# Performance work log

Hardware: AMD Instinct MI355X
Metric: run time of the kernel (lower is better)

The kernel has to match this reference:

```python
import jax, jax.numpy as jnp
import numpy as np

B, S, HID = 2, 4096, 3584
NH, NKV, HD, FD = 16, 8, 256, 64
CHUNK = 64

def _rope_tables(seq_len, dim, base=10000.0):
    inv = 1.0 / (base ** (np.arange(0, dim, 2) / dim))      # [dim/2]
    f = np.outer(np.arange(seq_len), inv)                   # [S, dim/2]
    return jnp.asarray(np.cos(f), jnp.float32), jnp.asarray(np.sin(f), jnp.float32)

def setup_inputs() -> dict:
    key = jax.random.key(0)
    ks = jax.random.split(key, 8)
    def w(k, shape, fan):
        return jax.random.normal(k, shape, jnp.float32) * (fan ** -0.5)
    cos, sin = _rope_tables(S, HD)
    return dict(
        hidden_states=jax.random.normal(ks[0], (B, S, HID), jnp.float32),
        cos=cos, sin=sin,
        Wq=w(ks[1], (HID, NH * HD), HID),
        Wk=w(ks[2], (HID, NKV * HD), HID),
        Wv=w(ks[3], (HID, NKV * HD), HID),
        Wo=w(ks[4], (NH * HD, HID), NH * HD),
        fmq=w(ks[5], (NH, HD, FD), HD),
        fmk=w(ks[6], (NH, HD, FD), HD),
    )

def apply_rope(x, cos, sin):
    # Gemma split-half rotary. x: [B,S,h,D]; cos/sin: [S,D/2]
    d2 = x.shape[-1] // 2
    x1, x2 = x[..., :d2], x[..., d2:]
    c = cos[None, :, None, :]
    s = sin[None, :, None, :]
    return jnp.concatenate([x1 * c - x2 * s, x1 * s + x2 * c], axis=-1)

def feature_map(x, w):
    # Hedgehog: per-head linear then cat(softmax(z), softmax(-z)).
    # x: [B,h,S,D], w: [h,D,F] -> [B,h,S,2F]
    z = jnp.einsum('bhsd,hdf->bhsf', x, w)
    return jnp.concatenate([jax.nn.softmax(z, axis=-1), jax.nn.softmax(-z, axis=-1)], axis=-1)

def chunk_linear_attn(q, k, v, chunk=CHUNK):
    # q,k: [B,H,T,dk]; v: [B,H,T,dv]; T divisible by chunk (S=4096, chunk=64)
    b, h, T, dk = q.shape
    dv = v.shape[-1]
    n = T // chunk
    q = q.reshape(b, h, n, chunk, dk) * (dk ** -0.5)
    k = k.reshape(b, h, n, chunk, dk)
    v = v.reshape(b, h, n, chunk, dv)
    kv = jnp.einsum('bhncd,bhnce->bhnde', k, v)          # per-chunk K^T V: [b,h,n,dk,dv]
    kv = jnp.cumsum(kv, axis=2)
    kv = jnp.concatenate([jnp.zeros_like(kv[:, :, :1]), kv[:, :, :-1]], axis=2)  # exclusive
    inter = jnp.einsum('bhncd,bhnde->bhnce', q, kv)
    scores = jnp.einsum('bhncd,bhnkd->bhnck', q, k)
    causal = jnp.tril(jnp.ones((chunk, chunk), dtype=bool))
    scores = jnp.where(causal, scores, jnp.zeros((), scores.dtype))
    intra = jnp.einsum('bhnck,bhnke->bhnce', scores, v)
    return (inter + intra).reshape(b, h, T, dv)

def reference(hidden_states, cos, sin, Wq, Wk, Wv, Wo, fmq, fmk):
    b, s, _ = hidden_states.shape
    q = (hidden_states @ Wq).reshape(b, s, NH, HD)
    k = (hidden_states @ Wk).reshape(b, s, NKV, HD)
    v = (hidden_states @ Wv).reshape(b, s, NKV, HD)
    q = apply_rope(q, cos, sin)
    k = apply_rope(k, cos, sin)
    g = NH // NKV
    k = jnp.repeat(k, g, axis=2)   # GQA expansion
    v = jnp.repeat(v, g, axis=2)
    q = q.transpose(0, 2, 1, 3)    # [B,H,S,D]
    k = k.transpose(0, 2, 1, 3)
    v = v.transpose(0, 2, 1, 3)
    q = feature_map(q, fmq)        # [B,H,S,2F]
    k = feature_map(k, fmk)
    o = chunk_linear_attn(q, k, v)                      # [B,H,S,HD]
    o = o.transpose(0, 2, 1, 3).reshape(b, s, NH * HD)
    return o @ Wo
```

## Files before the change

kernel.cpp:

```cpp
#include <hip/hip_runtime.h>

typedef float  f32x4  __attribute__((ext_vector_type(4)));
typedef __bf16 bf16x4 __attribute__((ext_vector_type(4)));
typedef __bf16 bf16x8 __attribute__((ext_vector_type(8)));

#define MFMA16(a,b,c) __builtin_amdgcn_mfma_f32_16x16x32_bf16((a),(b),(c),0,0,0)

__device__ __forceinline__ void async_copy16(void* lds, const void* gmem) {
  __builtin_amdgcn_global_load_lds(
      (const __attribute__((address_space(1))) void*)gmem,
      (__attribute__((address_space(3))) void*)lds, 16, 0, 0);
}

template<int N> __device__ __forceinline__ void vmcnt_gate() {
  if constexpr (N == 8) asm volatile("s_waitcnt vmcnt(8)" ::: "memory");
  else if constexpr (N == 4) asm volatile("s_waitcnt vmcnt(4)" ::: "memory");
  else if constexpr (N == 0) asm volatile("s_waitcnt vmcnt(0)" ::: "memory");
}

__global__ __launch_bounds__(256) void convert_kernel(const float* __restrict__ in,
                                                      __bf16* __restrict__ out, size_t n4) {
  size_t i = (size_t)blockIdx.x * 256 + threadIdx.x;
  if (i >= n4) return;
  f32x4 v = *(const f32x4*)(in + i * 4);
  bf16x4 o;
  #pragma unroll
  for (int j = 0; j < 4; ++j) o[j] = (__bf16)v[j];
  *(bf16x4*)(out + i * 4) = o;
}

__global__ __launch_bounds__(256) void transpose_kernel(const float* __restrict__ in,
                                                        __bf16* __restrict__ out, int R, int C) {
  __shared__ float tile[32][33];
  int bx = blockIdx.x, by = blockIdx.y;
  int tx = threadIdx.x & 31, ty0 = threadIdx.x >> 5;
  #pragma unroll
  for (int i = 0; i < 4; ++i) {
    int r = by * 32 + ty0 + i * 8;
    tile[ty0 + i * 8][tx] = in[(size_t)r * C + bx * 32 + tx];
  }
  __syncthreads();
  #pragma unroll
  for (int i = 0; i < 4; ++i) {
    int c = bx * 32 + ty0 + i * 8;
    out[(size_t)c * R + by * 32 + tx] = (__bf16)tile[tx][ty0 + i * 8];
  }
}


__device__ __forceinline__ void stage_q(__bf16* region, int qrow, const __bf16* src,
                                        int K, int w, int l) {
  int r = qrow + w * 8 + (l >> 3);
  async_copy16(region + (size_t)(qrow + w * 8) * 64,
               src + (size_t)r * K + (((l & 7) ^ (r & 7)) << 3));
}

#define PH_SYNC_PRE  do { asm volatile("s_barrier" ::: "memory"); \
                          asm volatile("s_waitcnt lgkmcnt(0)" ::: "memory"); \
                          __builtin_amdgcn_sched_barrier(0); \
                          __builtin_amdgcn_s_setprio(1); } while (0)
#define PH_SYNC_POST do { __builtin_amdgcn_s_setprio(0); \
                          __builtin_amdgcn_sched_barrier(0); } while (0)

template<bool LATE, bool EARLY, int GATE>
__device__ __forceinline__ void tile_body(__bf16* smem,
                                          const __bf16* Apan, const __bf16* Bpan,
                                          int K, int tau, int wm, int wn,
                                          int lo, int hi, int w, int l,
                                          f32x4 (&acc)[8][4]) {
  const int buf = tau & 1, nbuf = buf ^ 1;
  __bf16* Ab = smem + buf * 32768;
  __bf16* Bb = Ab + 16384;
  __bf16* An = smem + nbuf * 32768;
  __bf16* Bn = An + 16384;
  bf16x8 a[4], b[4];

  #pragma unroll
  for (int t = 0; t < 4; ++t) {
    int ra = wm * 128 + t * 16 + lo;
    a[t] = *(const bf16x8*)(Ab + (size_t)ra * 64 + ((hi ^ (ra & 7)) << 3));
  }
  #pragma unroll
  for (int t = 0; t < 4; ++t) {
    int rb = wn * 64 + t * 16 + lo;
    b[t] = *(const bf16x8*)(Bb + (size_t)rb * 64 + ((hi ^ (rb & 7)) << 3));
  }
  if constexpr (LATE) {
    const __bf16* Ap1 = Apan + (size_t)(tau + 1) * 64;
    const __bf16* Bp1 = Bpan + (size_t)(tau + 1) * 64;
    stage_q(An, 64,  Ap1, K, w, l);
    stage_q(An, 192, Ap1, K, w, l);
    stage_q(Bn, 128, Bp1, K, w, l);
    stage_q(Bn, 192, Bp1, K, w, l);
  }
  PH_SYNC_PRE;
  #pragma unroll
  for (int mt = 0; mt < 4; ++mt)
    #pragma unroll
    for (int nt = 0; nt < 4; ++nt)
      acc[mt][nt] = MFMA16(a[mt], b[nt], acc[mt][nt]);
  PH_SYNC_POST;
  asm volatile("s_barrier" ::: "memory");

  #pragma unroll
  for (int t = 0; t < 4; ++t) {
    int ra = wm * 128 + 64 + t * 16 + lo;
    a[t] = *(const bf16x8*)(Ab + (size_t)ra * 64 + ((hi ^ (ra & 7)) << 3));
  }
  PH_SYNC_PRE;
  #pragma unroll
  for (int mt = 0; mt < 4; ++mt)
    #pragma unroll
    for (int nt = 0; nt < 4; ++nt)
      acc[4 + mt][nt] = MFMA16(a[mt], b[nt], acc[4 + mt][nt]);
  PH_SYNC_POST;
  asm volatile("s_barrier" ::: "memory");

  #pragma unroll
  for (int t = 0; t < 4; ++t) {
    int ra = wm * 128 + t * 16 + lo;
    a[t] = *(const bf16x8*)(Ab + (size_t)ra * 64 + (((4 + hi) ^ (ra & 7)) << 3));
  }
  #pragma unroll
  for (int t = 0; t < 4; ++t) {
    int rb = wn * 64 + t * 16 + lo;
    b[t] = *(const bf16x8*)(Bb + (size_t)rb * 64 + (((4 + hi) ^ (rb & 7)) << 3));
  }
  PH_SYNC_PRE;
  #pragma unroll
  for (int mt = 0; mt < 4; ++mt)
    #pragma unroll
    for (int nt = 0; nt < 4; ++nt)
      acc[mt][nt] = MFMA16(a[mt], b[nt], acc[mt][nt]);
  PH_SYNC_POST;
  asm volatile("s_barrier" ::: "memory");

  #pragma unroll
  for (int t = 0; t < 4; ++t) {
    int ra = wm * 128 + 64 + t * 16 + lo;
    a[t] = *(const bf16x8*)(Ab + (size_t)ra * 64 + (((4 + hi) ^ (ra & 7)) << 3));
  }
  if constexpr (EARLY) {
    const __bf16* Ap2 = Apan + (size_t)(tau + 2) * 64;
    const __bf16* Bp2 = Bpan + (size_t)(tau + 2) * 64;
    stage_q(Ab, 0,   Ap2, K, w, l);
    stage_q(Ab, 128, Ap2, K, w, l);
    stage_q(Bb, 0,   Bp2, K, w, l);
    stage_q(Bb, 64,  Bp2, K, w, l);
  }
  PH_SYNC_PRE;
  #pragma unroll
  for (int mt = 0; mt < 4; ++mt)
    #pragma unroll
    for (int nt = 0; nt < 4; ++nt)
      acc[4 + mt][nt] = MFMA16(a[mt], b[nt], acc[4 + mt][nt]);
  PH_SYNC_POST;
  vmcnt_gate<GATE>();
  asm volatile("s_barrier" ::: "memory");
}

template <typename CT>
__global__ __launch_bounds__(512) void gemm256_kernel(const __bf16* __restrict__ A,
                                                      const __bf16* __restrict__ Bt,
                                                      CT* __restrict__ C, int M, int N, int K) {
  extern __shared__ __bf16 smem[];

  const int gx = gridDim.x;
  const int nwg = gx * gridDim.y;
  const int wg = blockIdx.y * gx + blockIdx.x;
  const int qq = nwg >> 3;
  const int id2 = (wg & 7) * qq + (wg >> 3);
  const int m0 = (id2 / gx) * 256, n0 = (id2 % gx) * 256;

  const int tid = threadIdx.x;
  const int l = tid & 63, w = tid >> 6;
  const int lo = l & 15, hi = l >> 4;
  const int wm = w >> 2, wn = w & 3;

  const __bf16* Apan = A + (size_t)m0 * K;
  const __bf16* Bpan = Bt + (size_t)n0 * K;

  f32x4 acc[8][4] = {};

  #pragma unroll
  for (int q = 0; q < 4; ++q) stage_q(smem,          q * 64, Apan,      K, w, l);
  #pragma unroll
  for (int q = 0; q < 4; ++q) stage_q(smem + 16384,  q * 64, Bpan,      K, w, l);
  #pragma unroll
  for (int q = 0; q < 4; ++q) stage_q(smem + 32768,  q * 64, Apan + 64, K, w, l);
  #pragma unroll
  for (int q = 0; q < 4; ++q) stage_q(smem + 49152,  q * 64, Bpan + 64, K, w, l);
  asm volatile("s_waitcnt vmcnt(8)" ::: "memory");
  asm volatile("s_barrier" ::: "memory");

  const int T = K >> 6;
  tile_body<false, true, 4>(smem, Apan, Bpan, K, 0, wm, wn, lo, hi, w, l, acc);
  for (int tau = 1; tau < T - 2; ++tau)
    tile_body<true, true, 4>(smem, Apan, Bpan, K, tau, wm, wn, lo, hi, w, l, acc);
  tile_body<true, false, 0>(smem, Apan, Bpan, K, T - 2, wm, wn, lo, hi, w, l, acc);
  tile_body<false, false, -1>(smem, Apan, Bpan, K, T - 1, wm, wn, lo, hi, w, l, acc);

  #pragma unroll
  for (int mt = 0; mt < 8; ++mt)
    #pragma unroll
    for (int nt = 0; nt < 4; ++nt) {
      int col = n0 + wn * 64 + nt * 16 + lo;
      #pragma unroll
      for (int r = 0; r < 4; ++r) {
        int row = m0 + wm * 128 + mt * 16 + 4 * hi + r;
        C[(size_t)row * N + col] = (CT)acc[mt][nt][r];
      }
    }
}

__global__ __launch_bounds__(256) void rope_kernel(const __bf16* __restrict__ qin,
                                                   const float* __restrict__ cosT,
                                                   const float* __restrict__ sinT,
                                                   __bf16* __restrict__ outp, int H, int bshift) {
  int idx = blockIdx.x * 256 + threadIdx.x;
  int j = idx & 31;
  int s = (idx >> 5) & 4095;
  int h = (idx >> 17) & (H - 1);
  int b = idx >> bshift;
  int d = j * 4;
  size_t ibase = ((size_t)(b * 4096 + s)) * (H * 256) + h * 256 + d;
  bf16x4 x1 = *(const bf16x4*)&qin[ibase];
  bf16x4 x2 = *(const bf16x4*)&qin[ibase + 128];
  f32x4 c  = *(const f32x4*)&cosT[s * 128 + d];
  f32x4 sn = *(const f32x4*)&sinT[s * 128 + d];
  bf16x4 o1, o2;
  #pragma unroll
  for (int t = 0; t < 4; ++t) {
    float a = (float)x1[t], bb = (float)x2[t];
    o1[t] = (__bf16)(a * c[t] - bb * sn[t]);
    o2[t] = (__bf16)(a * sn[t] + bb * c[t]);
  }
  size_t obase = (((size_t)(b * H + h)) * 4096 + s) * 256 + d;
  *(bf16x4*)&outp[obase] = o1;
  *(bf16x4*)&outp[obase + 128] = o2;
}

__global__ __launch_bounds__(256) void vperm_kernel(const __bf16* __restrict__ in,
                                                    __bf16* __restrict__ out) {
  int idx = blockIdx.x * 256 + threadIdx.x;
  int j = idx & 31;
  int s = (idx >> 5) & 4095;
  int kv = (idx >> 17) & 7;
  int b = idx >> 20;
  bf16x8 v = *(const bf16x8*)&in[((size_t)(b * 4096 + s)) * 2048 + kv * 256 + j * 8];
  *(bf16x8*)&out[(((size_t)(b * 8 + kv)) * 4096 + s) * 256 + j * 8] = v;
}

__global__ __launch_bounds__(256) void fm_kernel(const __bf16* __restrict__ rope,
                                                 const float* __restrict__ fm,
                                                 __bf16* __restrict__ out, int srcH, float scale) {
  __shared__ __bf16 fmT[64][256];
  int bh = blockIdx.y;
  int h = bh & 15, b = bh >> 4;
  int s0 = blockIdx.x * 128;
  int tid = threadIdx.x, lane = tid & 63, wid = tid >> 6, hi = lane >> 4, lo = lane & 15;

  const float* fmh = fm + (size_t)h * 256 * 64;
  for (int i = tid; i < 256 * 64; i += 256) {
    int d = i >> 6, f = i & 63;
    fmT[f][(((d >> 3) ^ (f & 7)) << 3) | (d & 7)] = (__bf16)fmh[i];
  }
  __syncthreads();

  int srch = (srcH == 16) ? h : (h >> 1);
  const __bf16* abase = rope + ((size_t)(b * srcH + srch) * 4096 + s0 + 32 * wid) * 256;
  f32x4 acc[2][4] = {};
  for (int kk = 0; kk < 256; kk += 32) {
    bf16x8 a[2], bf[4];
    #pragma unroll
    for (int mt = 0; mt < 2; ++mt)
      a[mt] = *(const bf16x8*)(abase + (size_t)(16 * mt + lo) * 256 + kk + 8 * hi);
    const int G = (kk >> 3) + hi;
    #pragma unroll
    for (int nt = 0; nt < 4; ++nt) {
      int f = 16 * nt + lo;
      bf[nt] = *(const bf16x8*)&fmT[f][(G ^ (f & 7)) << 3];
    }
    #pragma unroll
    for (int mt = 0; mt < 2; ++mt)
      #pragma unroll
      for (int nt = 0; nt < 4; ++nt)
        acc[mt][nt] = MFMA16(a[mt], bf[nt], acc[mt][nt]);
  }

  size_t obase = ((size_t)(b * 16 + h) * 4096 + s0 + 32 * wid);
  #pragma unroll
  for (int mt = 0; mt < 2; ++mt) {
    #pragma unroll
    for (int r = 0; r < 4; ++r) {
      float z0 = acc[mt][0][r], z1 = acc[mt][1][r], z2 = acc[mt][2][r], z3 = acc[mt][3][r];
      float mx = fmaxf(fmaxf(z0, z1), fmaxf(z2, z3));
      float mn = fminf(fminf(z0, z1), fminf(z2, z3));
      #pragma unroll
      for (int off = 1; off < 16; off <<= 1) {
        mx = fmaxf(mx, __shfl_xor(mx, off));
        mn = fminf(mn, __shfl_xor(mn, off));
      }
      float ep0 = __expf(z0 - mx), ep1 = __expf(z1 - mx), ep2 = __expf(z2 - mx), ep3 = __expf(z3 - mx);
      float en0 = __expf(mn - z0), en1 = __expf(mn - z1), en2 = __expf(mn - z2), en3 = __expf(mn - z3);
      float sp = ep0 + ep1 + ep2 + ep3, sn = en0 + en1 + en2 + en3;
      #pragma unroll
      for (int off = 1; off < 16; off <<= 1) {
        sp += __shfl_xor(sp, off);
        sn += __shfl_xor(sn, off);
      }
      float rp = scale / sp, rn = scale / sn;
      int row = 16 * mt + 4 * hi + r;
      __bf16* op = out + (obase + row) * 128;
      op[0  + lo] = (__bf16)(ep0 * rp);  op[16 + lo] = (__bf16)(ep1 * rp);
      op[32 + lo] = (__bf16)(ep2 * rp);  op[48 + lo] = (__bf16)(ep3 * rp);
      op[64 + lo] = (__bf16)(en0 * rn);  op[80 + lo] = (__bf16)(en1 * rn);
      op[96 + lo] = (__bf16)(en2 * rn);  op[112 + lo] = (__bf16)(en3 * rn);
    }
  }
}

__global__ __launch_bounds__(256) void attn_kernel(const __bf16* __restrict__ qf,
                                                   const __bf16* __restrict__ kf,
                                                   const __bf16* __restrict__ vp,
                                                   __bf16* __restrict__ o) {
  __shared__ __bf16 k_s[64][128];
  __shared__ __bf16 vT_s[32][64];
  __shared__ __bf16 sc_s[64][64];
  __shared__ __bf16 STb[32][128];

  int bid = blockIdx.x;
  int dvb = bid & 7, h = (bid >> 3) & 15, b = bid >> 7;
  int dv0 = dvb * 32;
  int tid = threadIdx.x, lane = tid & 63, wid = tid >> 6, hi = lane >> 4, lo = lane & 15;

  const __bf16* qh = qf + ((size_t)(b * 16 + h)) * 4096 * 128;
  const __bf16* kh = kf + ((size_t)(b * 16 + h)) * 4096 * 128;
  const __bf16* vh = vp + ((size_t)(b * 8 + (h >> 1))) * 4096 * 256 + dv0;
  __bf16* oh = o + ((size_t)b * 4096) * 4096 + h * 256 + dv0;

  {
    unsigned int* z = (unsigned int*)&STb[0][0];
    for (int i = tid; i < 2048; i += 256) z[i] = 0u;
  }
  f32x4 st[2][2] = {};

  for (int n = 0; n < 64; ++n) {
    int s0 = n * 64;
    #pragma unroll
    for (int i = 0; i < 4; ++i) {
      int rb = (wid * 4 + i) * 4;
      int r = rb + (lane >> 4);
      int Glog = (lane & 15) ^ (r & 7);
      async_copy16(&k_s[rb][0], kh + (size_t)(s0 + r) * 128 + Glog * 8);
    }
    {
      int c = tid >> 2, d8 = (tid & 3) * 8;
      bf16x8 vv = *(const bf16x8*)(vh + (size_t)(s0 + c) * 256 + d8);
      #pragma unroll
      for (int j = 0; j < 8; ++j) {
        int dv = d8 + j;
        vT_s[dv][(((c >> 3) ^ (dv & 7)) << 3) | (c & 7)] = vv[j];
      }
    }
    __syncthreads();

    bf16x8 aq[4];
    #pragma unroll
    for (int kq = 0; kq < 4; ++kq)
      aq[kq] = *(const bf16x8*)(qh + (size_t)(s0 + 16 * wid + lo) * 128 + 32 * kq + 8 * hi);

    f32x4 acc_o[2] = {}, sacc[4] = {};
    #pragma unroll
    for (int nt = 0; nt < 2; ++nt)
      #pragma unroll
      for (int kq = 0; kq < 4; ++kq) {
        int rr = 16 * nt + lo, G = 4 * kq + hi;
        bf16x8 bf = *(const bf16x8*)&STb[rr][(G ^ (rr & 7)) << 3];
        acc_o[nt] = MFMA16(aq[kq], bf, acc_o[nt]);
      }
    #pragma unroll
    for (int nt = 0; nt < 4; ++nt)
      #pragma unroll
      for (int kq = 0; kq < 4; ++kq) {
        int rr = 16 * nt + lo, G = 4 * kq + hi;
        bf16x8 bf = *(const bf16x8*)&k_s[rr][(G ^ (rr & 7)) << 3];
        sacc[nt] = MFMA16(aq[kq], bf, sacc[nt]);
      }
    #pragma unroll
    for (int nt = 0; nt < 4; ++nt)
      #pragma unroll
      for (int r = 0; r < 4; ++r) {
        int c = 16 * wid + 4 * hi + r;
        int cp = 16 * nt + lo;
        float v = (cp <= c) ? sacc[nt][r] : 0.0f;
        sc_s[c][(((cp >> 3) ^ (c & 7)) << 3) | (cp & 7)] = (__bf16)v;
      }
    asm volatile("" ::: "memory");
    #pragma unroll
    for (int nt = 0; nt < 2; ++nt)
      #pragma unroll
      for (int kq = 0; kq < 2; ++kq) {
        int rA = 16 * wid + lo, GA = 4 * kq + hi;
        bf16x8 af = *(const bf16x8*)&sc_s[rA][(GA ^ (rA & 7)) << 3];
        int rB = 16 * nt + lo;
        bf16x8 bf = *(const bf16x8*)&vT_s[rB][(GA ^ (rB & 7)) << 3];
        acc_o[nt] = MFMA16(af, bf, acc_o[nt]);
      }
    #pragma unroll
    for (int nt = 0; nt < 2; ++nt)
      #pragma unroll
      for (int r = 0; r < 4; ++r) {
        int c = 16 * wid + 4 * hi + r;
        oh[(size_t)(s0 + c) * 4096 + 16 * nt + lo] = (__bf16)acc_o[nt][r];
      }
    __syncthreads();

    bf16x8 bu[2][2];
    #pragma unroll
    for (int q = 0; q < 2; ++q) {
      int dk = 16 * (2 * wid + q) + lo;
      #pragma unroll
      for (int kq = 0; kq < 2; ++kq) {
        bf16x8 tmp;
        #pragma unroll
        for (int j = 0; j < 8; ++j) {
          int c = 32 * kq + 8 * hi + j;
          tmp[j] = k_s[c][(((dk >> 3) ^ (c & 7)) << 3) | (dk & 7)];
        }
        bu[q][kq] = tmp;
      }
    }
    #pragma unroll
    for (int mt = 0; mt < 2; ++mt)
      #pragma unroll
      for (int kq = 0; kq < 2; ++kq) {
        int rA = 16 * mt + lo, GA = 4 * kq + hi;
        bf16x8 av = *(const bf16x8*)&vT_s[rA][(GA ^ (rA & 7)) << 3];
        #pragma unroll
        for (int q = 0; q < 2; ++q)
          st[mt][q] = MFMA16(av, bu[q][kq], st[mt][q]);
      }
    #pragma unroll
    for (int mt = 0; mt < 2; ++mt)
      #pragma unroll
      for (int q = 0; q < 2; ++q) {
        int dk = 16 * (2 * wid + q) + lo;
        #pragma unroll
        for (int r = 0; r < 4; ++r) {
          int dvr = 16 * mt + 4 * hi + r;
          STb[dvr][(((dk >> 3) ^ (dvr & 7)) << 3) | (dk & 7)] = (__bf16)st[mt][q][r];
        }
      }
    __syncthreads();
  }
}

extern "C" void kernel_launch(void* const* d_in, const int* in_sizes, int n_in,
                              void* d_out, int out_size, void* d_ws, size_t ws_size,
                              hipStream_t stream) {
  (void)in_sizes; (void)n_in; (void)out_size; (void)ws_size;
  const float* hs   = (const float*)d_in[0];
  const float* cosT = (const float*)d_in[1];
  const float* sinT = (const float*)d_in[2];
  const float* Wq   = (const float*)d_in[3];
  const float* Wk   = (const float*)d_in[4];
  const float* Wv   = (const float*)d_in[5];
  const float* Wo   = (const float*)d_in[6];
  const float* fmq  = (const float*)d_in[7];
  const float* fmk  = (const float*)d_in[8];
  float* out = (float*)d_out;
  char* ws = (char*)d_ws;

  hipFuncSetAttribute((const void*)gemm256_kernel<__bf16>,
                      hipFuncAttributeMaxDynamicSharedMemorySize, 131072);
  hipFuncSetAttribute((const void*)gemm256_kernel<float>,
                      hipFuncAttributeMaxDynamicSharedMemorySize, 131072);

  const size_t MB = 1024ull * 1024ull;
  __bf16* Xb   = (__bf16*)(ws + 0);
  __bf16* ropq = (__bf16*)(ws + 0);
  __bf16* Wqt  = (__bf16*)(ws + 70 * MB);
  __bf16* ropk = (__bf16*)(ws + 70 * MB);
  __bf16* Wkt  = (__bf16*)(ws + 104 * MB);
  __bf16* vpb  = (__bf16*)(ws + 104 * MB);
  __bf16* Wvt  = (__bf16*)(ws + 119 * MB);
  __bf16* Wot  = (__bf16*)(ws + 140 * MB);
  __bf16* Qb   = (__bf16*)(ws + 170 * MB);
  __bf16* ob   = (__bf16*)(ws + 170 * MB);
  __bf16* Kb   = (__bf16*)(ws + 238 * MB);
  __bf16* qfb  = (__bf16*)(ws + 238 * MB);
  __bf16* Vb   = (__bf16*)(ws + 272 * MB);
  __bf16* kfb  = (__bf16*)(ws + 272 * MB);

  convert_kernel<<<28672, 256, 0, stream>>>(hs, Xb, (size_t)8192 * 3584 / 4);
  transpose_kernel<<<dim3(128, 112), 256, 0, stream>>>(Wq, Wqt, 3584, 4096);
  transpose_kernel<<<dim3(64, 112),  256, 0, stream>>>(Wk, Wkt, 3584, 2048);
  transpose_kernel<<<dim3(64, 112),  256, 0, stream>>>(Wv, Wvt, 3584, 2048);
  transpose_kernel<<<dim3(112, 128), 256, 0, stream>>>(Wo, Wot, 4096, 3584);

  gemm256_kernel<__bf16><<<dim3(16, 32), 512, 131072, stream>>>(Xb, Wqt, Qb, 8192, 4096, 3584);
  gemm256_kernel<__bf16><<<dim3(8, 32),  512, 131072, stream>>>(Xb, Wkt, Kb, 8192, 2048, 3584);
  gemm256_kernel<__bf16><<<dim3(8, 32),  512, 131072, stream>>>(Xb, Wvt, Vb, 8192, 2048, 3584);

  rope_kernel<<<16384, 256, 0, stream>>>(Qb, cosT, sinT, ropq, 16, 21);
  rope_kernel<<<8192, 256, 0, stream>>>(Kb, cosT, sinT, ropk, 8, 20);
  vperm_kernel<<<8192, 256, 0, stream>>>(Vb, vpb);

  fm_kernel<<<dim3(32, 32), 256, 0, stream>>>(ropq, fmq, qfb, 16, 0.08838834764831845f);
  fm_kernel<<<dim3(32, 32), 256, 0, stream>>>(ropk, fmk, kfb, 8, 1.0f);

  attn_kernel<<<256, 256, 0, stream>>>(qfb, kfb, vpb, ob);

  gemm256_kernel<float><<<dim3(14, 32), 512, 131072, stream>>>(ob, Wot, out, 8192, 3584, 4096);
}
```

Measured before the change: 1.004 ms.

## Restructure GEMM main loop to prefetch LDS fragments across phases and tiles

Reworks the 256x256 bf16 GEMM tile body so A/B register fragments are loaded one phase ahead, including the first fragments of the next K-tile, and carried across iterations. It drops the extra barrier and lgkmcnt(0) wait before each MFMA block, regroups which B rows are staged early versus late, and moves vmcnt gates to new points. It also adds a min-blocks hint to launch_bounds. The aim is to hide LDS read latency and cut barrier stalls around the MFMA blocks. In exchange it raises register pressure from the extra fragment buffers and relies on subtle wait-count ordering for correctness.

```diff
diff --git a/kernel.cpp b/kernel.cpp
--- a/kernel.cpp
+++ b/kernel.cpp
@@ -14,7 +14,9 @@
 
 template<int N> __device__ __forceinline__ void vmcnt_gate() {
   if constexpr (N == 8) asm volatile("s_waitcnt vmcnt(8)" ::: "memory");
+  else if constexpr (N == 6) asm volatile("s_waitcnt vmcnt(6)" ::: "memory");
   else if constexpr (N == 4) asm volatile("s_waitcnt vmcnt(4)" ::: "memory");
+  else if constexpr (N == 2) asm volatile("s_waitcnt vmcnt(2)" ::: "memory");
   else if constexpr (N == 0) asm volatile("s_waitcnt vmcnt(0)" ::: "memory");
 }
 
@@ -55,90 +57,83 @@
                src + (size_t)r * K + (((l & 7) ^ (r & 7)) << 3));
 }
 
-#define PH_SYNC_PRE  do { asm volatile("s_barrier" ::: "memory"); \
-                          asm volatile("s_waitcnt lgkmcnt(0)" ::: "memory"); \
-                          __builtin_amdgcn_sched_barrier(0); \
-                          __builtin_amdgcn_s_setprio(1); } while (0)
-#define PH_SYNC_POST do { __builtin_amdgcn_s_setprio(0); \
-                          __builtin_amdgcn_sched_barrier(0); } while (0)
-
-template<bool LATE, bool EARLY, int GATE>
+#define MFMA_PRE  do { __builtin_amdgcn_sched_barrier(0); \
+                       __builtin_amdgcn_s_setprio(1); } while (0)
+#define MFMA_POST do { __builtin_amdgcn_s_setprio(0); \
+                       __builtin_amdgcn_sched_barrier(0); } while (0)
+
+template<bool LATE, bool EARLY, bool NEXT, int G2, int G3>
 __device__ __forceinline__ void tile_body(__bf16* smem,
                                           const __bf16* Apan, const __bf16* Bpan,
                                           int K, int tau, int wm, int wn,
                                           int lo, int hi, int w, int l,
+                                          bf16x8 (&aA)[4], bf16x8 (&aB)[4], bf16x8 (&b)[4],
                                           f32x4 (&acc)[8][4]) {
   const int buf = tau & 1, nbuf = buf ^ 1;
   __bf16* Ab = smem + buf * 32768;
   __bf16* Bb = Ab + 16384;
   __bf16* An = smem + nbuf * 32768;
   __bf16* Bn = An + 16384;
-  bf16x8 a[4], b[4];
-
-  #pragma unroll
-  for (int t = 0; t < 4; ++t) {
-    int ra = wm * 128 + t * 16 + lo;
-    a[t] = *(const bf16x8*)(Ab + (size_t)ra * 64 + ((hi ^ (ra & 7)) << 3));
-  }
-  #pragma unroll
-  for (int t = 0; t < 4; ++t) {
-    int rb = wn * 64 + t * 16 + lo;
-    b[t] = *(const bf16x8*)(Bb + (size_t)rb * 64 + ((hi ^ (rb & 7)) << 3));
+
+  #pragma unroll
+  for (int t = 0; t < 4; ++t) {
+    int ra = wm * 128 + 64 + t * 16 + lo;
+    aB[t] = *(const bf16x8*)(Ab + (size_t)ra * 64 + ((hi ^ (ra & 7)) << 3));
   }
   if constexpr (LATE) {
     const __bf16* Ap1 = Apan + (size_t)(tau + 1) * 64;
-    const __bf16* Bp1 = Bpan + (size_t)(tau + 1) * 64;
     stage_q(An, 64,  Ap1, K, w, l);
     stage_q(An, 192, Ap1, K, w, l);
-    stage_q(Bn, 128, Bp1, K, w, l);
-    stage_q(Bn, 192, Bp1, K, w, l);
-  }
-  PH_SYNC_PRE;
+  }
+  MFMA_PRE;
   #pragma unroll
   for (int mt = 0; mt < 4; ++mt)
     #pragma unroll
     for (int nt = 0; nt < 4; ++nt)
-      acc[mt][nt] = MFMA16(a[mt], b[nt], acc[mt][nt]);
-  PH_SYNC_POST;
+      acc[mt][nt] = MFMA16(aA[mt], b[nt], acc[mt][nt]);
+  MFMA_POST;
   asm volatile("s_barrier" ::: "memory");
 
   #pragma unroll
   for (int t = 0; t < 4; ++t) {
-    int ra = wm * 128 + 64 + t * 16 + lo;
-    a[t] = *(const bf16x8*)(Ab + (size_t)ra * 64 + ((hi ^ (ra & 7)) << 3));
-  }
-  PH_SYNC_PRE;
+    int ra = wm * 128 + t * 16 + lo;
+    aA[t] = *(const bf16x8*)(Ab + (size_t)ra * 64 + (((4 + hi) ^ (ra & 7)) << 3));
+  }
+  MFMA_PRE;
   #pragma unroll
   for (int mt = 0; mt < 4; ++mt)
     #pragma unroll
     for (int nt = 0; nt < 4; ++nt)
-      acc[4 + mt][nt] = MFMA16(a[mt], b[nt], acc[4 + mt][nt]);
-  PH_SYNC_POST;
-  asm volatile("s_barrier" ::: "memory");
-
-  #pragma unroll
-  for (int t = 0; t < 4; ++t) {
-    int ra = wm * 128 + t * 16 + lo;
-    a[t] = *(const bf16x8*)(Ab + (size_t)ra * 64 + (((4 + hi) ^ (ra & 7)) << 3));
-  }
+      acc[4 + mt][nt] = MFMA16(aB[mt], b[nt], acc[4 + mt][nt]);
+  MFMA_POST;
   #pragma unroll
   for (int t = 0; t < 4; ++t) {
     int rb = wn * 64 + t * 16 + lo;
     b[t] = *(const bf16x8*)(Bb + (size_t)rb * 64 + (((4 + hi) ^ (rb & 7)) << 3));
   }
-  PH_SYNC_PRE;
+  asm volatile("s_barrier" ::: "memory");
+
+  #pragma unroll
+  for (int t = 0; t < 4; ++t) {
+    int ra = wm * 128 + 64 + t * 16 + lo;
+    aB[t] = *(const bf16x8*)(Ab + (size_t)ra * 64 + (((4 + hi) ^ (ra & 7)) << 3));
+  }
+  MFMA_PRE;
   #pragma unroll
   for (int mt = 0; mt < 4; ++mt)
     #pragma unroll
     for (int nt = 0; nt < 4; ++nt)
-      acc[mt][nt] = MFMA16(a[mt], b[nt], acc[mt][nt]);
-  PH_SYNC_POST;
+      acc[mt][nt] = MFMA16(aA[mt], b[nt], acc[mt][nt]);
+  MFMA_POST;
+  if constexpr (G2 >= 0) vmcnt_gate<G2>();
   asm volatile("s_barrier" ::: "memory");
 
-  #pragma unroll
-  for (int t = 0; t < 4; ++t) {
-    int ra = wm * 128 + 64 + t * 16 + lo;
-    a[t] = *(const bf16x8*)(Ab + (size_t)ra * 64 + (((4 + hi) ^ (ra & 7)) << 3));
+  if constexpr (NEXT) {
+    #pragma unroll
+    for (int t = 0; t < 4; ++t) {
+      int ra = wm * 128 + t * 16 + lo;
+      aA[t] = *(const bf16x8*)(An + (size_t)ra * 64 + ((hi ^ (ra & 7)) << 3));
+    }
   }
   if constexpr (EARLY) {
     const __bf16* Ap2 = Apan + (size_t)(tau + 2) * 64;
@@ -147,22 +142,31 @@
     stage_q(Ab, 128, Ap2, K, w, l);
     stage_q(Bb, 0,   Bp2, K, w, l);
     stage_q(Bb, 64,  Bp2, K, w, l);
-  }
-  PH_SYNC_PRE;
+    stage_q(Bb, 128, Bp2, K, w, l);
+    stage_q(Bb, 192, Bp2, K, w, l);
+  }
+  MFMA_PRE;
   #pragma unroll
   for (int mt = 0; mt < 4; ++mt)
     #pragma unroll
     for (int nt = 0; nt < 4; ++nt)
-      acc[4 + mt][nt] = MFMA16(a[mt], b[nt], acc[4 + mt][nt]);
-  PH_SYNC_POST;
-  vmcnt_gate<GATE>();
+      acc[4 + mt][nt] = MFMA16(aB[mt], b[nt], acc[4 + mt][nt]);
+  MFMA_POST;
+  if constexpr (NEXT) {
+    #pragma unroll
+    for (int t = 0; t < 4; ++t) {
+      int rb = wn * 64 + t * 16 + lo;
+      b[t] = *(const bf16x8*)(Bn + (size_t)rb * 64 + ((hi ^ (rb & 7)) << 3));
+    }
+  }
+  if constexpr (G3 >= 0) vmcnt_gate<G3>();
   asm volatile("s_barrier" ::: "memory");
 }
 
 template <typename CT>
-__global__ __launch_bounds__(512) void gemm256_kernel(const __bf16* __restrict__ A,
-                                                      const __bf16* __restrict__ Bt,
-                                                      CT* __restrict__ C, int M, int N, int K) {
+__global__ __launch_bounds__(512, 2) void gemm256_kernel(const __bf16* __restrict__ A,
+                                                         const __bf16* __restrict__ Bt,
+                                                         CT* __restrict__ C, int M, int N, int K) {
   extern __shared__ __bf16 smem[];
 
   const int gx = gridDim.x;
@@ -181,24 +185,44 @@
   const __bf16* Bpan = Bt + (size_t)n0 * K;
 
   f32x4 acc[8][4] = {};
-
-  #pragma unroll
-  for (int q = 0; q < 4; ++q) stage_q(smem,          q * 64, Apan,      K, w, l);
-  #pragma unroll
-  for (int q = 0; q < 4; ++q) stage_q(smem + 16384,  q * 64, Bpan,      K, w, l);
-  #pragma unroll
-  for (int q = 0; q < 4; ++q) stage_q(smem + 32768,  q * 64, Apan + 64, K, w, l);
-  #pragma unroll
-  for (int q = 0; q < 4; ++q) stage_q(smem + 49152,  q * 64, Bpan + 64, K, w, l);
-  asm volatile("s_waitcnt vmcnt(8)" ::: "memory");
+  bf16x8 aA[4], aB[4], b[4];
+
+  stage_q(smem,          0,   Apan, K, w, l);
+  stage_q(smem,          128, Apan, K, w, l);
+  stage_q(smem + 16384,  0,   Bpan, K, w, l);
+  stage_q(smem + 16384,  64,  Bpan, K, w, l);
+  stage_q(smem + 16384,  128, Bpan, K, w, l);
+  stage_q(smem + 16384,  192, Bpan, K, w, l);
+  stage_q(smem,          64,  Apan, K, w, l);
+  stage_q(smem,          192, Apan, K, w, l);
+  stage_q(smem + 32768,  0,   Apan + 64, K, w, l);
+  stage_q(smem + 32768,  128, Apan + 64, K, w, l);
+  stage_q(smem + 49152,  0,   Bpan + 64, K, w, l);
+  stage_q(smem + 49152,  64,  Bpan + 64, K, w, l);
+  stage_q(smem + 49152,  128, Bpan + 64, K, w, l);
+  stage_q(smem + 49152,  192, Bpan + 64, K, w, l);
+  stage_q(smem + 32768,  64,  Apan + 64, K, w, l);
+  stage_q(smem + 32768,  192, Apan + 64, K, w, l);
+  vmcnt_gate<8>();
   asm volatile("s_barrier" ::: "memory");
 
+  #pragma unroll
+  for (int t = 0; t < 4; ++t) {
+    int ra = wm * 128 + t * 16 + lo;
+    aA[t] = *(const bf16x8*)(smem + (size_t)ra * 64 + ((hi ^ (ra & 7)) << 3));
+  }
+  #pragma unroll
+  for (int t = 0; t < 4; ++t) {
+    int rb = wn * 64 + t * 16 + lo;
+    b[t] = *(const bf16x8*)(smem + 16384 + (size_t)rb * 64 + ((hi ^ (rb & 7)) << 3));
+  }
+
   const int T = K >> 6;
-  tile_body<false, true, 4>(smem, Apan, Bpan, K, 0, wm, wn, lo, hi, w, l, acc);
+  tile_body<false, true,  true,  2,  6>(smem, Apan, Bpan, K, 0,     wm, wn, lo, hi, w, l, aA, aB, b, acc);
   for (int tau = 1; tau < T - 2; ++tau)
-    tile_body<true, true, 4>(smem, Apan, Bpan, K, tau, wm, wn, lo, hi, w, l, acc);
-  tile_body<true, false, 0>(smem, Apan, Bpan, K, T - 2, wm, wn, lo, hi, w, l, acc);
-  tile_body<false, false, -1>(smem, Apan, Bpan, K, T - 1, wm, wn, lo, hi, w, l, acc);
+    tile_body<true, true,  true,  2,  6>(smem, Apan, Bpan, K, tau,   wm, wn, lo, hi, w, l, aA, aB, b, acc);
+  tile_body<true,  false, true,  2,  0>(smem, Apan, Bpan, K, T - 2, wm, wn, lo, hi, w, l, aA, aB, b, acc);
+  tile_body<false, false, false, -1, -1>(smem, Apan, Bpan, K, T - 1, wm, wn, lo, hi, w, l, aA, aB, b, acc);
 
   #pragma unroll
   for (int mt = 0; mt < 8; ++mt)
```

After: 977.9 us. 2.6% less time.
